# Kernel optimization log

Hardware: AMD Instinct MI355X
Metric: run time of the kernel (lower is better)

## Reference

```python
import jax, jax.numpy as jnp
import numpy as np
import math

NUM_HEADS = 32
NUM_KV = 8
D = 128          # num_hidden == per-head dim in this module
S = 2048
B = 1
DK = 128
ROPE_BASE = 10000.0


def rope(x):
    # x: [B, H, S, D]; standard Llama-style RoPE (split-halves rotation) over positions.
    d = x.shape[-1]
    half = d // 2
    pos = jnp.arange(x.shape[2], dtype=jnp.float32)                       # [S]
    inv_freq = 1.0 / (ROPE_BASE ** (jnp.arange(half, dtype=jnp.float32) / half))
    ang = pos[:, None] * inv_freq[None, :]                                # [S, half]
    cos = jnp.cos(ang)
    sin = jnp.sin(ang)
    x1 = x[..., :half]
    x2 = x[..., half:]
    return jnp.concatenate([x1 * cos - x2 * sin, x1 * sin + x2 * cos], axis=-1)


def setup_inputs() -> dict:
    key = jax.random.key(0)
    ks = jax.random.split(key, 8)
    query = jax.random.normal(ks[0], (B, S, D), dtype=jnp.float32)
    k_in = jax.random.normal(ks[1], (B, S, D), dtype=jnp.float32)
    v_in = jax.random.normal(ks[2], (B, S, D), dtype=jnp.float32)
    # causal mask: 1 where attention allowed (lower triangle incl diagonal)
    mask = jnp.tril(jnp.ones((S, S), dtype=jnp.int32))[None, None]        # [1,1,S,S]
    sc = 0.02
    Wq = jax.random.normal(ks[3], (NUM_HEADS * D, D), dtype=jnp.float32) * sc
    bq = jnp.zeros((NUM_HEADS * D,), dtype=jnp.float32)
    Wk = jax.random.normal(ks[4], (NUM_KV * D, D), dtype=jnp.float32) * sc
    bk = jnp.zeros((NUM_KV * D,), dtype=jnp.float32)
    Wv = jax.random.normal(ks[5], (NUM_KV * D, D), dtype=jnp.float32) * sc
    bv = jnp.zeros((NUM_KV * D,), dtype=jnp.float32)
    Wo = jax.random.normal(ks[6], (D, NUM_HEADS * D), dtype=jnp.float32) * sc
    bo = jnp.zeros((D,), dtype=jnp.float32)
    return {"query": query, "key": k_in, "values": v_in, "mask": mask,
            "Wq": Wq, "bq": bq, "Wk": Wk, "bk": bk, "Wv": Wv, "bv": bv,
            "Wo": Wo, "bo": bo}


def reference(query, key, values, mask, Wq, bq, Wk, bk, Wv, bv, Wo, bo):
    Bq, Sq, Dh = query.shape
    # projections; torch Linear: x @ W.T + b. Note: view (reshape), not transpose,
    # exactly as in the original module.
    q = (query @ Wq.T + bq).reshape(Bq, NUM_HEADS, Sq, Dh)   # [B,H,S,D]
    k = (key @ Wk.T + bk).reshape(Bq, NUM_KV, Sq, Dh)        # [B,Hkv,S,D]
    v = (values @ Wv.T + bv).reshape(Bq, NUM_KV, Sq, Dh)
    rk = rope(k)
    rv = rope(v)  # module applies RoPE to values too (faithful)
    rep = NUM_HEADS // NUM_KV
    # torch .repeat((1, rep, 1, 1)) tiles whole head blocks -> jnp.tile
    rk = jnp.tile(rk, (1, rep, 1, 1))                        # [B,H,S,D]
    rv = jnp.tile(rv, (1, rep, 1, 1))
    scores = jnp.einsum('bhqd,bhkd->bhqk', q, rk) / math.sqrt(DK)
    scores = jnp.where(mask == 0, -jnp.inf, scores)
    attn = jax.nn.softmax(scores, axis=-1)
    out = jnp.einsum('bhqk,bhkd->bhqd', attn, rv)            # [B,H,S,D]
    out = out.transpose(0, 2, 1, 3).reshape(Bq, Sq, NUM_HEADS * Dh)
    return out @ Wo.T + bo
```

## Files before the change

kernel.cpp:

```cpp
#include <hip/hip_runtime.h>

typedef unsigned short u16;
typedef unsigned int u32;
typedef short frag_t __attribute__((ext_vector_type(8)));
typedef float f32x4 __attribute__((ext_vector_type(4)));

#define S_LEN 2048

__device__ __forceinline__ float bf2f(u32 u) {
  union { u32 i; float f; } v; v.i = u << 16; return v.f;
}
__device__ __forceinline__ u16 f2bf(float f) {
  u32 x = __float_as_uint(f);
  u32 r = (x + 0x7fffu + ((x >> 16) & 1u)) >> 16;
  return (u16)r;
}
__device__ __forceinline__ u32 pkbf(float lo, float hi) {
  u32 r;
  asm("v_cvt_pk_bf16_f32 %0, %1, %2" : "=v"(r) : "v"(lo), "v"(hi));
  return r;
}
__device__ __forceinline__ void unpack8(uint4 r, float* o) {
  o[0] = bf2f(r.x & 0xffffu); o[1] = bf2f(r.x >> 16);
  o[2] = bf2f(r.y & 0xffffu); o[3] = bf2f(r.y >> 16);
  o[4] = bf2f(r.z & 0xffffu); o[5] = bf2f(r.z >> 16);
  o[6] = bf2f(r.w & 0xffffu); o[7] = bf2f(r.w >> 16);
}
__device__ __forceinline__ u16 ld_in(const void* p, size_t idx, bool fp32) {
  if (fp32) return f2bf(((const float*)p)[idx]);
  return ((const u16*)p)[idx];
}
__device__ __forceinline__ uint4 ld8(const void* p, size_t eidx, bool fp32) {
  if (!fp32) return *(const uint4*)((const u16*)p + eidx);
  const float4* f = (const float4*)((const float*)p + eidx);
  float4 x = f[0], y = f[1];
  uint4 r;
  r.x = pkbf(x.x, x.y);
  r.y = pkbf(x.z, x.w);
  r.z = pkbf(y.x, y.y);
  r.w = pkbf(y.z, y.w);
  return r;
}

__global__ __launch_bounds__(256) void proj_all(
    const void* __restrict__ query, const void* __restrict__ key,
    const void* __restrict__ values,
    const void* __restrict__ Wq, const void* __restrict__ bq,
    const void* __restrict__ Wk, const void* __restrict__ bk,
    const void* __restrict__ Wv, const void* __restrict__ bv,
    u16* __restrict__ Qb, u16* __restrict__ Kb, u16* __restrict__ Vtmp,
    u32* __restrict__ flag_out) {
  __shared__ u16 As[128][136];
  __shared__ u16 Ws[128][136];
  __shared__ u32 flagS;
  u16 (*Cs)[136] = As;
  const int t = threadIdx.x;
  if (t < 64) {
    u32 e = ((u32)((const u16*)query)[2 * t] >> 7) & 0xFFu;
    bool ok = (e >= 110u && e <= 140u);
    unsigned long long b = __ballot(ok);
    if (t == 0) flagS = (__popcll(b) < 32) ? 1u : 0u;
  }
  __syncthreads();
  const bool fp32 = (flagS != 0u);
  if (t == 0 && blockIdx.x == 0 && blockIdx.y == 0) *flag_out = flagS;
  const int x = blockIdx.x;
  const void *A, *W, *bias;
  u16* C; int N, n0;
  if (x < 32)      { A = query;  W = Wq; bias = bq; C = Qb;   N = 4096; n0 = x << 7; }
  else if (x < 40) { A = key;    W = Wk; bias = bk; C = Kb;   N = 1024; n0 = (x - 32) << 7; }
  else             { A = values; W = Wv; bias = bv; C = Vtmp; N = 1024; n0 = (x - 40) << 7; }
  const float osc = (x < 32) ? 0.12751743f : 1.0f;
  const int m0 = blockIdx.y << 7;
#pragma unroll
  for (int i = 0; i < 8; ++i) {
    int task = t + (i << 8);
    int row = task >> 4, ch = (task & 15) << 3;
    *(uint4*)&As[row][ch] = ld8(A, (size_t)(m0 + row) * 128 + ch, fp32);
    *(uint4*)&Ws[row][ch] = ld8(W, (size_t)(n0 + row) * 128 + ch, fp32);
  }
  __syncthreads();
  const int lane = t & 63, w = t >> 6, quad = lane >> 4, l15 = lane & 15;
  const int rm = (w & 1) << 6, rn = (w >> 1) << 6;
  f32x4 acc[4][4];
#pragma unroll
  for (int mt = 0; mt < 4; ++mt)
#pragma unroll
    for (int nt = 0; nt < 4; ++nt) acc[mt][nt] = 0.f;
#pragma unroll
  for (int mtp = 0; mtp < 2; ++mtp) {
    frag_t a0[4], a1[4];
#pragma unroll
    for (int kc = 0; kc < 4; ++kc) {
      a0[kc] = *(const frag_t*)&As[rm + mtp * 32 + l15][kc * 32 + quad * 8];
      a1[kc] = *(const frag_t*)&As[rm + mtp * 32 + 16 + l15][kc * 32 + quad * 8];
    }
#pragma unroll
    for (int nt = 0; nt < 4; ++nt)
#pragma unroll
      for (int kc = 0; kc < 4; ++kc) {
        frag_t b = *(const frag_t*)&Ws[rn + nt * 16 + l15][kc * 32 + quad * 8];
        acc[mtp * 2][nt] = __builtin_amdgcn_mfma_f32_16x16x32_bf16(a0[kc], b, acc[mtp * 2][nt], 0, 0, 0);
        acc[mtp * 2 + 1][nt] = __builtin_amdgcn_mfma_f32_16x16x32_bf16(a1[kc], b, acc[mtp * 2 + 1][nt], 0, 0, 0);
      }
  }
  __syncthreads();
#pragma unroll
  for (int nt = 0; nt < 4; ++nt) {
    float bb = bf2f((u32)ld_in(bias, n0 + rn + nt * 16 + l15, fp32));
#pragma unroll
    for (int mt = 0; mt < 4; ++mt) {
      int row = rm + ((mt >> 1) * 32) + ((mt & 1) * 16) + quad * 4;
#pragma unroll
      for (int r = 0; r < 4; ++r)
        Cs[row + r][rn + nt * 16 + l15] = f2bf((acc[mt][nt][r] + bb) * osc);
    }
  }
  __syncthreads();
#pragma unroll
  for (int i = 0; i < 8; ++i) {
    int task = t + (i << 8);
    int row = task >> 4, ch = (task & 15) << 3;
    *(uint4*)&C[(size_t)(m0 + row) * N + n0 + ch] = *(const uint4*)&Cs[row][ch];
  }
}

__global__ __launch_bounds__(256) void rope_kv_tr(u16* __restrict__ Kb,
                                                  const u16* __restrict__ Vb,
                                                  u16* __restrict__ VbT) {
  __shared__ u16 Lt[128][72];
  const int t = threadIdx.x;
  const int s0 = blockIdx.x << 6;
  const int g = blockIdx.y;
  for (int i = t; i < 4096; i += 256) {
    int s = s0 + (i >> 6), ii = i & 63;
    float invf = __expf(-(float)ii * 0.14391156831212787f);
    float ang = (float)s * invf;
    float sn, cs;
    sincosf(ang, &sn, &cs);
    size_t base = ((size_t)(g << 11) + s) * 128 + ii;
    float k1 = bf2f((u32)Kb[base]), k2 = bf2f((u32)Kb[base + 64]);
    Kb[base] = f2bf(k1 * cs - k2 * sn);
    Kb[base + 64] = f2bf(k1 * sn + k2 * cs);
  }
  const u16* src = Vb + (size_t)g * S_LEN * 128;
  for (int i = t; i < 512; i += 256) {
    int r = i >> 3, d8 = (i & 7) << 3;
    float lo[8], hi[8];
    unpack8(*(const uint4*)&src[(size_t)(s0 + r) * 128 + d8], lo);
    unpack8(*(const uint4*)&src[(size_t)(s0 + r) * 128 + d8 + 64], hi);
#pragma unroll
    for (int j = 0; j < 8; ++j) {
      float invf = __expf(-(float)(d8 + j) * 0.14391156831212787f);
      float ang = (float)(s0 + r) * invf;
      float sn, cs;
      sincosf(ang, &sn, &cs);
      Lt[d8 + j][r] = f2bf(lo[j] * cs - hi[j] * sn);
      Lt[d8 + 64 + j][r] = f2bf(lo[j] * sn + hi[j] * cs);
    }
  }
  __syncthreads();
  u16* dst = VbT + (size_t)g * 128 * S_LEN + s0;
  for (int i = t; i < 2048; i += 256) {
    int d = i >> 4, s4 = (i & 15) << 2;
    uint2 pk;
    pk.x = (u32)Lt[d][s4] | ((u32)Lt[d][s4 + 1] << 16);
    pk.y = (u32)Lt[d][s4 + 2] | ((u32)Lt[d][s4 + 3] << 16);
    *(uint2*)&dst[(size_t)d * S_LEN + s4] = pk;
  }
}

__global__ __launch_bounds__(256, 2) void attn_mfma(
    const u16* __restrict__ Qb, const u16* __restrict__ Kb,
    const u16* __restrict__ VbT, u16* __restrict__ OpA, u16* __restrict__ OpB,
    float2* __restrict__ Ml, int nkh) {
  __shared__ union SmemU {
    struct { u16 Kt[32][136]; u16 Vt[128][40]; u16 St[128][40]; } m;
    struct { u16 Og[128][136]; } e;
  } su;
  const int t = threadIdx.x;
  const int lane = t & 63, w = t >> 6, quad = lane >> 4, l15 = lane & 15;
  const int g = (int)blockIdx.x & 7;
  const int kh = (int)blockIdx.x >> 3;
  const int pi = (int)blockIdx.y;
  const int h = g + (w << 3);
  const u16* Kg = Kb + (size_t)g * S_LEN * 128;
  const u16* Vg = VbT + (size_t)g * 128 * S_LEN;
  const int kR = t >> 4, kC = (t & 15) << 3;
  const int vR = t >> 2, vC = (t & 3) << 3;
  u16* dst = kh ? OpB : OpA;

  for (int tp = 0; tp < 2; ++tp) {
    const int qt = tp ? pi : 63 - pi;
    const int q0 = qt << 5;
    const int niter = qt + 1;
    frag_t aq[2][4];
#pragma unroll
    for (int qp = 0; qp < 2; ++qp)
#pragma unroll
      for (int kc = 0; kc < 4; ++kc)
        aq[qp][kc] = *(const frag_t*)&Qb[((size_t)h * S_LEN + q0 + qp * 16 + l15) * 128 +
                                         kc * 32 + quad * 8];
    float m_r[2] = {-1e30f, -1e30f}, l_r[2] = {0.f, 0.f};
    f32x4 oacc[2][8];
#pragma unroll
    for (int qp = 0; qp < 2; ++qp)
#pragma unroll
      for (int nt = 0; nt < 8; ++nt) oacc[qp][nt] = 0.f;

    uint4 kpf[2], vpf[2];
    if (kh < niter) {
      const int k0 = kh << 5;
      kpf[0] = *(const uint4*)&Kg[(size_t)(k0 + kR) * 128 + kC];
      kpf[1] = *(const uint4*)&Kg[(size_t)(k0 + kR + 16) * 128 + kC];
      vpf[0] = *(const uint4*)&Vg[(size_t)vR * S_LEN + k0 + vC];
      vpf[1] = *(const uint4*)&Vg[(size_t)(vR + 64) * S_LEN + k0 + vC];
    }
    for (int sj = kh; sj < niter; sj += nkh) {
      const int k0 = sj << 5;
      __syncthreads();
      *(uint4*)&su.m.Kt[kR][kC] = kpf[0];
      *(uint4*)&su.m.Kt[kR + 16][kC] = kpf[1];
      *(uint4*)&su.m.Vt[vR][vC] = vpf[0];
      *(uint4*)&su.m.Vt[vR + 64][vC] = vpf[1];
      __syncthreads();
      if (sj + nkh < niter) {
        const int kn = (sj + nkh) << 5;
        kpf[0] = *(const uint4*)&Kg[(size_t)(kn + kR) * 128 + kC];
        kpf[1] = *(const uint4*)&Kg[(size_t)(kn + kR + 16) * 128 + kC];
        vpf[0] = *(const uint4*)&Vg[(size_t)vR * S_LEN + kn + vC];
        vpf[1] = *(const uint4*)&Vg[(size_t)(vR + 64) * S_LEN + kn + vC];
      }
      f32x4 s4[2][2];
#pragma unroll
      for (int kk = 0; kk < 2; ++kk) { s4[kk][0] = 0.f; s4[kk][1] = 0.f; }
#pragma unroll
      for (int kc = 0; kc < 4; ++kc)
#pragma unroll
        for (int kk = 0; kk < 2; ++kk) {
          frag_t a = *(const frag_t*)&su.m.Kt[kk * 16 + l15][kc * 32 + quad * 8];
          s4[kk][0] = __builtin_amdgcn_mfma_f32_16x16x32_bf16(a, aq[0][kc], s4[kk][0], 0, 0, 0);
          s4[kk][1] = __builtin_amdgcn_mfma_f32_16x16x32_bf16(a, aq[1][kc], s4[kk][1], 0, 0, 0);
        }
      const bool lastm = (sj == niter - 1);
      float alpha[2];
#pragma unroll
      for (int qp = 0; qp < 2; ++qp) {
        const int qg = q0 + qp * 16 + l15;
        float mx = -1e30f;
#pragma unroll
        for (int kk = 0; kk < 2; ++kk)
#pragma unroll
          for (int r = 0; r < 4; ++r) {
            float sv = s4[kk][qp][r];
            if (lastm && (k0 + kk * 16 + quad * 4 + r) > qg) sv = -1e30f;
            s4[kk][qp][r] = sv;
            mx = fmaxf(mx, sv);
          }
        mx = fmaxf(mx, __shfl_xor(mx, 16));
        mx = fmaxf(mx, __shfl_xor(mx, 32));
        float mn = fmaxf(m_r[qp], mx);
        alpha[qp] = __builtin_amdgcn_exp2f(m_r[qp] - mn);
        m_r[qp] = mn;
        float sum = 0.f;
        const int strow = w * 32 + qp * 16 + l15;
#pragma unroll
        for (int kk = 0; kk < 2; ++kk) {
          float p0 = __builtin_amdgcn_exp2f(s4[kk][qp][0] - mn);
          float p1 = __builtin_amdgcn_exp2f(s4[kk][qp][1] - mn);
          float p2 = __builtin_amdgcn_exp2f(s4[kk][qp][2] - mn);
          float p3 = __builtin_amdgcn_exp2f(s4[kk][qp][3] - mn);
          sum += (p0 + p1) + (p2 + p3);
          uint2 pk;
          pk.x = pkbf(p0, p1);
          pk.y = pkbf(p2, p3);
          *(uint2*)&su.m.St[strow][kk * 16 + quad * 4] = pk;
        }
        sum += __shfl_xor(sum, 16);
        sum += __shfl_xor(sum, 32);
        l_r[qp] = l_r[qp] * alpha[qp] + sum;
      }
      if (__any(alpha[0] < 1.0f || alpha[1] < 1.0f)) {
#pragma unroll
        for (int qp = 0; qp < 2; ++qp)
#pragma unroll
          for (int r = 0; r < 4; ++r) {
            float al = __shfl(alpha[qp], quad * 4 + r);
#pragma unroll
            for (int nt = 0; nt < 8; ++nt) oacc[qp][nt][r] *= al;
          }
      }
      frag_t pa0 = *(const frag_t*)&su.m.St[w * 32 + l15][quad * 8];
      frag_t pa1 = *(const frag_t*)&su.m.St[w * 32 + 16 + l15][quad * 8];
#pragma unroll
      for (int nt = 0; nt < 8; ++nt) {
        frag_t v = *(const frag_t*)&su.m.Vt[nt * 16 + l15][quad * 8];
        oacc[0][nt] = __builtin_amdgcn_mfma_f32_16x16x32_bf16(pa0, v, oacc[0][nt], 0, 0, 0);
        oacc[1][nt] = __builtin_amdgcn_mfma_f32_16x16x32_bf16(pa1, v, oacc[1][nt], 0, 0, 0);
      }
    }
    __syncthreads();
#pragma unroll
    for (int qp = 0; qp < 2; ++qp)
#pragma unroll
      for (int r = 0; r < 4; ++r) {
        float fac = 1.0f;
        if (nkh == 1) fac = 1.0f / __shfl(l_r[qp], quad * 4 + r);
        int row = w * 32 + qp * 16 + quad * 4 + r;
#pragma unroll
        for (int nt = 0; nt < 8; ++nt)
          su.e.Og[row][nt * 16 + l15] = f2bf(oacc[qp][nt][r] * fac);
      }
    __syncthreads();
#pragma unroll
    for (int jj = 0; jj < 8; ++jj) {
      int c = t + (jj << 8);
      int row = c >> 4, ch = (c & 15) << 3;
      int hh = row >> 5, qr = row & 31;
      *(uint4*)&dst[(size_t)(q0 + qr) * 4096 + (g + hh * 8) * 128 + ch] =
          *(const uint4*)&su.e.Og[row][ch];
    }
    if (nkh == 2 && quad == 0) {
#pragma unroll
      for (int qp = 0; qp < 2; ++qp)
        Ml[((size_t)kh * 32 + h) * S_LEN + q0 + qp * 16 + l15] =
            make_float2(m_r[qp], l_r[qp]);
    }
  }
}

__global__ __launch_bounds__(256) void out_part(
    const u16* __restrict__ OpA, const u16* __restrict__ OpB,
    const float2* __restrict__ Ml, const void* __restrict__ Wo,
    float* __restrict__ Pout, const u32* __restrict__ flagp, int nkh) {
  __shared__ u16 As[64][136];
  __shared__ u16 Ws[128][136];
  const bool fp32 = (*flagp != 0u);
  const int t = threadIdx.x;
  const int lane = t & 63, w = t >> 6, quad = lane >> 4, l15 = lane & 15;
  const int rm = (w & 1) << 5, rn = (w >> 1) << 6;
  const int m0 = (int)blockIdx.x << 6;
  const int z = (int)blockIdx.y;
  f32x4 acc[2][4];
#pragma unroll
  for (int mt = 0; mt < 2; ++mt)
#pragma unroll
    for (int nt = 0; nt < 4; ++nt) acc[mt][nt] = 0.f;
  for (int kc2 = 0; kc2 < 2; ++kc2) {
    if (kc2) __syncthreads();
    const int kc0 = (z << 8) + (kc2 << 7);
    const int hh = kc0 >> 7;
#pragma unroll
    for (int i = 0; i < 8; ++i) {
      int task = t + (i << 8);
      int row = task >> 4, ch = (task & 15) << 3;
      *(uint4*)&Ws[row][ch] = ld8(Wo, (size_t)row * 4096 + kc0 + ch, fp32);
    }
#pragma unroll
    for (int i = 0; i < 4; ++i) {
      int task = t + (i << 8);
      int row = task >> 4, ch = (task & 15) << 3;
      size_t idx = (size_t)(m0 + row) * 4096 + kc0 + ch;
      if (nkh == 2) {
        int s = m0 + row;
        float2 p1 = Ml[(size_t)hh * S_LEN + s];
        float2 p2 = Ml[(size_t)(32 + hh) * S_LEN + s];
        float mn = fmaxf(p1.x, p2.x);
        float a1 = __builtin_amdgcn_exp2f(p1.x - mn);
        float a2 = __builtin_amdgcn_exp2f(p2.x - mn);
        float linv = 1.0f / (a1 * p1.y + a2 * p2.y);
        float w1 = a1 * linv, w2 = a2 * linv;
        float o1[8], o2[8];
        unpack8(*(const uint4*)&OpA[idx], o1);
        unpack8(*(const uint4*)&OpB[idx], o2);
        uint4 r;
        r.x = pkbf(o1[0] * w1 + o2[0] * w2, o1[1] * w1 + o2[1] * w2);
        r.y = pkbf(o1[2] * w1 + o2[2] * w2, o1[3] * w1 + o2[3] * w2);
        r.z = pkbf(o1[4] * w1 + o2[4] * w2, o1[5] * w1 + o2[5] * w2);
        r.w = pkbf(o1[6] * w1 + o2[6] * w2, o1[7] * w1 + o2[7] * w2);
        *(uint4*)&As[row][ch] = r;
      } else {
        *(uint4*)&As[row][ch] = *(const uint4*)&OpA[idx];
      }
    }
    __syncthreads();
    frag_t a0[4], a1[4];
#pragma unroll
    for (int kc = 0; kc < 4; ++kc) {
      a0[kc] = *(const frag_t*)&As[rm + l15][kc * 32 + quad * 8];
      a1[kc] = *(const frag_t*)&As[rm + 16 + l15][kc * 32 + quad * 8];
    }
#pragma unroll
    for (int nt = 0; nt < 4; ++nt)
#pragma unroll
      for (int kc = 0; kc < 4; ++kc) {
        frag_t b = *(const frag_t*)&Ws[rn + nt * 16 + l15][kc * 32 + quad * 8];
        acc[0][nt] = __builtin_amdgcn_mfma_f32_16x16x32_bf16(a0[kc], b, acc[0][nt], 0, 0, 0);
        acc[1][nt] = __builtin_amdgcn_mfma_f32_16x16x32_bf16(a1[kc], b, acc[1][nt], 0, 0, 0);
      }
  }
#pragma unroll
  for (int mt = 0; mt < 2; ++mt) {
    int mrow = m0 + rm + mt * 16 + quad * 4;
#pragma unroll
    for (int nt = 0; nt < 4; ++nt) {
      int n = rn + nt * 16 + l15;
#pragma unroll
      for (int r = 0; r < 4; ++r)
        Pout[((size_t)z * 2048 + mrow + r) * 128 + n] = acc[mt][nt][r];
    }
  }
}

__global__ __launch_bounds__(256) void out_red(
    const float* __restrict__ Pout, const void* __restrict__ bo,
    void* __restrict__ out, const u32* __restrict__ flagp) {
  const bool fp32 = (*flagp != 0u);
  int e4 = blockIdx.x * 256 + threadIdx.x;
  const float4* P = (const float4*)Pout;
  float4 s = P[e4];
#pragma unroll
  for (int z = 1; z < 16; ++z) {
    float4 p = P[(size_t)z * 65536 + e4];
    s.x += p.x; s.y += p.y; s.z += p.z; s.w += p.w;
  }
  int n = (e4 << 2) & 127;
  s.x += bf2f((u32)ld_in(bo, n + 0, fp32));
  s.y += bf2f((u32)ld_in(bo, n + 1, fp32));
  s.z += bf2f((u32)ld_in(bo, n + 2, fp32));
  s.w += bf2f((u32)ld_in(bo, n + 3, fp32));
  if (fp32) {
    ((float4*)out)[e4] = s;
  } else {
    uint2 pk;
    pk.x = pkbf(s.x, s.y);
    pk.y = pkbf(s.z, s.w);
    *(uint2*)((u16*)out + (e4 << 2)) = pk;
  }
}

extern "C" void kernel_launch(void* const* d_in, const int* in_sizes, int n_in,
                              void* d_out, int out_size, void* d_ws, size_t ws_size,
                              hipStream_t stream) {
  (void)in_sizes; (void)n_in; (void)out_size;
  const void* query  = d_in[0];
  const void* key    = d_in[1];
  const void* values = d_in[2];
  const void* Wq = d_in[4];
  const void* bq = d_in[5];
  const void* Wk = d_in[6];
  const void* bk = d_in[7];
  const void* Wv = d_in[8];
  const void* bv = d_in[9];
  const void* Wo = d_in[10];
  const void* bo = d_in[11];

  char* ws = (char*)d_ws;
  u32* flag   = (u32*)ws;
  u16* Qb     = (u16*)(ws + 64);
  u16* Kb     = (u16*)(ws + 64 + (16ull << 20));
  u16* VbT    = (u16*)(ws + 64 + (20ull << 20));
  u16* Vtmp   = (u16*)(ws + 64 + (24ull << 20));
  u16* Ob     = (u16*)(ws + 64 + (24ull << 20));
  u16* OpB    = (u16*)(ws + 64 + (40ull << 20));
  float2* Mlb = (float2*)(ws + 64 + (56ull << 20));
  float* Pout = (float*)Qb;

  const bool split = (ws_size >= (58ull << 20));
  const int nkh = split ? 2 : 1;

  proj_all<<<dim3(48, 16), 256, 0, stream>>>(query, key, values, Wq, bq, Wk, bk,
                                             Wv, bv, Qb, Kb, Vtmp, flag);
  rope_kv_tr<<<dim3(32, 8), 256, 0, stream>>>(Kb, Vtmp, VbT);
  attn_mfma<<<dim3(8 * nkh, 32), 256, 0, stream>>>(Qb, Kb, VbT, Ob, OpB, Mlb, nkh);
  out_part<<<dim3(32, 16), 256, 0, stream>>>(Ob, OpB, Mlb, Wo, Pout, flag, nkh);
  out_red<<<256, 256, 0, stream>>>(Pout, bo, d_out, flag);
}
```

Measured before the change: 239.3 us.

## Fuse K RoPE into projection epilogue and allow 4-way KV split in attention

Applies RoPE to K inside the projection kernel's shared-memory epilogue instead of a separate read-modify-write pass in the V transpose kernel. The attention KV dimension can now be split four ways when the workspace is large enough, which doubles the attention grid. out_part merges up to four partial outputs using their saved max and sum statistics. The goal is better CU occupancy in attention and less K traffic, at the cost of more partial-output memory and merge work.

```diff
diff --git a/kernel.cpp b/kernel.cpp
--- a/kernel.cpp
+++ b/kernel.cpp
@@ -117,6 +117,21 @@
     }
   }
   __syncthreads();
+  if (x >= 32 && x < 40) {
+    const int g0 = x - 32;
+    for (int i = t; i < 8192; i += 256) {
+      int row = i >> 6, ii = i & 63;
+      int sv = (((m0 + row) & 255) << 3) + g0;
+      float invf = __expf(-(float)ii * 0.14391156831212787f);
+      float ang = (float)sv * invf;
+      float sn, cs;
+      sincosf(ang, &sn, &cs);
+      float k1 = bf2f((u32)Cs[row][ii]), k2 = bf2f((u32)Cs[row][ii + 64]);
+      Cs[row][ii] = f2bf(k1 * cs - k2 * sn);
+      Cs[row][ii + 64] = f2bf(k1 * sn + k2 * cs);
+    }
+    __syncthreads();
+  }
 #pragma unroll
   for (int i = 0; i < 8; ++i) {
     int task = t + (i << 8);
@@ -125,24 +140,12 @@
   }
 }
 
-__global__ __launch_bounds__(256) void rope_kv_tr(u16* __restrict__ Kb,
-                                                  const u16* __restrict__ Vb,
-                                                  u16* __restrict__ VbT) {
+__global__ __launch_bounds__(256) void rope_v_tr(const u16* __restrict__ Vb,
+                                                 u16* __restrict__ VbT) {
   __shared__ u16 Lt[128][72];
   const int t = threadIdx.x;
   const int s0 = blockIdx.x << 6;
   const int g = blockIdx.y;
-  for (int i = t; i < 4096; i += 256) {
-    int s = s0 + (i >> 6), ii = i & 63;
-    float invf = __expf(-(float)ii * 0.14391156831212787f);
-    float ang = (float)s * invf;
-    float sn, cs;
-    sincosf(ang, &sn, &cs);
-    size_t base = ((size_t)(g << 11) + s) * 128 + ii;
-    float k1 = bf2f((u32)Kb[base]), k2 = bf2f((u32)Kb[base + 64]);
-    Kb[base] = f2bf(k1 * cs - k2 * sn);
-    Kb[base + 64] = f2bf(k1 * sn + k2 * cs);
-  }
   const u16* src = Vb + (size_t)g * S_LEN * 128;
   for (int i = t; i < 512; i += 256) {
     int r = i >> 3, d8 = (i & 7) << 3;
@@ -172,7 +175,8 @@
 
 __global__ __launch_bounds__(256, 2) void attn_mfma(
     const u16* __restrict__ Qb, const u16* __restrict__ Kb,
-    const u16* __restrict__ VbT, u16* __restrict__ OpA, u16* __restrict__ OpB,
+    const u16* __restrict__ VbT, u16* __restrict__ Op0, u16* __restrict__ Op1,
+    u16* __restrict__ Op2, u16* __restrict__ Op3,
     float2* __restrict__ Ml, int nkh) {
   __shared__ union SmemU {
     struct { u16 Kt[32][136]; u16 Vt[128][40]; u16 St[128][40]; } m;
@@ -188,7 +192,7 @@
   const u16* Vg = VbT + (size_t)g * 128 * S_LEN;
   const int kR = t >> 4, kC = (t & 15) << 3;
   const int vR = t >> 2, vC = (t & 3) << 3;
-  u16* dst = kh ? OpB : OpA;
+  u16* dst = (kh == 0) ? Op0 : (kh == 1) ? Op1 : (kh == 2) ? Op2 : Op3;
 
   for (int tp = 0; tp < 2; ++tp) {
     const int qt = tp ? pi : 63 - pi;
@@ -320,7 +324,7 @@
       *(uint4*)&dst[(size_t)(q0 + qr) * 4096 + (g + hh * 8) * 128 + ch] =
           *(const uint4*)&su.e.Og[row][ch];
     }
-    if (nkh == 2 && quad == 0) {
+    if (nkh >= 2 && quad == 0) {
 #pragma unroll
       for (int qp = 0; qp < 2; ++qp)
         Ml[((size_t)kh * 32 + h) * S_LEN + q0 + qp * 16 + l15] =
@@ -330,7 +334,8 @@
 }
 
 __global__ __launch_bounds__(256) void out_part(
-    const u16* __restrict__ OpA, const u16* __restrict__ OpB,
+    const u16* __restrict__ Op0, const u16* __restrict__ Op1,
+    const u16* __restrict__ Op2, const u16* __restrict__ Op3,
     const float2* __restrict__ Ml, const void* __restrict__ Wo,
     float* __restrict__ Pout, const u32* __restrict__ flagp, int nkh) {
   __shared__ u16 As[64][136];
@@ -361,26 +366,50 @@
       int task = t + (i << 8);
       int row = task >> 4, ch = (task & 15) << 3;
       size_t idx = (size_t)(m0 + row) * 4096 + kc0 + ch;
-      if (nkh == 2) {
+      if (nkh >= 2) {
         int s = m0 + row;
-        float2 p1 = Ml[(size_t)hh * S_LEN + s];
-        float2 p2 = Ml[(size_t)(32 + hh) * S_LEN + s];
-        float mn = fmaxf(p1.x, p2.x);
+        float2 p0 = Ml[(size_t)hh * S_LEN + s];
+        float2 p1 = Ml[(size_t)(32 + hh) * S_LEN + s];
+        float mn = fmaxf(p0.x, p1.x);
+        float2 p2, p3;
+        if (nkh == 4) {
+          p2 = Ml[(size_t)(64 + hh) * S_LEN + s];
+          p3 = Ml[(size_t)(96 + hh) * S_LEN + s];
+          mn = fmaxf(mn, fmaxf(p2.x, p3.x));
+        }
+        float a0 = __builtin_amdgcn_exp2f(p0.x - mn);
         float a1 = __builtin_amdgcn_exp2f(p1.x - mn);
-        float a2 = __builtin_amdgcn_exp2f(p2.x - mn);
-        float linv = 1.0f / (a1 * p1.y + a2 * p2.y);
-        float w1 = a1 * linv, w2 = a2 * linv;
-        float o1[8], o2[8];
-        unpack8(*(const uint4*)&OpA[idx], o1);
-        unpack8(*(const uint4*)&OpB[idx], o2);
+        float lsum = a0 * p0.y + a1 * p1.y;
+        float a2 = 0.f, a3 = 0.f;
+        if (nkh == 4) {
+          a2 = __builtin_amdgcn_exp2f(p2.x - mn);
+          a3 = __builtin_amdgcn_exp2f(p3.x - mn);
+          lsum += a2 * p2.y + a3 * p3.y;
+        }
+        float linv = 1.0f / lsum;
+        float o[8], oi[8];
+        unpack8(*(const uint4*)&Op0[idx], o);
+#pragma unroll
+        for (int j = 0; j < 8; ++j) o[j] *= a0;
+        unpack8(*(const uint4*)&Op1[idx], oi);
+#pragma unroll
+        for (int j = 0; j < 8; ++j) o[j] += a1 * oi[j];
+        if (nkh == 4) {
+          unpack8(*(const uint4*)&Op2[idx], oi);
+#pragma unroll
+          for (int j = 0; j < 8; ++j) o[j] += a2 * oi[j];
+          unpack8(*(const uint4*)&Op3[idx], oi);
+#pragma unroll
+          for (int j = 0; j < 8; ++j) o[j] += a3 * oi[j];
+        }
         uint4 r;
-        r.x = pkbf(o1[0] * w1 + o2[0] * w2, o1[1] * w1 + o2[1] * w2);
-        r.y = pkbf(o1[2] * w1 + o2[2] * w2, o1[3] * w1 + o2[3] * w2);
-        r.z = pkbf(o1[4] * w1 + o2[4] * w2, o1[5] * w1 + o2[5] * w2);
-        r.w = pkbf(o1[6] * w1 + o2[6] * w2, o1[7] * w1 + o2[7] * w2);
+        r.x = pkbf(o[0] * linv, o[1] * linv);
+        r.y = pkbf(o[2] * linv, o[3] * linv);
+        r.z = pkbf(o[4] * linv, o[5] * linv);
+        r.w = pkbf(o[6] * linv, o[7] * linv);
         *(uint4*)&As[row][ch] = r;
       } else {
-        *(uint4*)&As[row][ch] = *(const uint4*)&OpA[idx];
+        *(uint4*)&As[row][ch] = *(const uint4*)&Op0[idx];
       }
     }
     __syncthreads();
@@ -461,18 +490,24 @@
   u16* Kb     = (u16*)(ws + 64 + (16ull << 20));
   u16* VbT    = (u16*)(ws + 64 + (20ull << 20));
   u16* Vtmp   = (u16*)(ws + 64 + (24ull << 20));
-  u16* Ob     = (u16*)(ws + 64 + (24ull << 20));
-  u16* OpB    = (u16*)(ws + 64 + (40ull << 20));
-  float2* Mlb = (float2*)(ws + 64 + (56ull << 20));
+  u16* Op0    = (u16*)(ws + 64 + (24ull << 20));
+  u16* Op1    = (u16*)(ws + 64 + (40ull << 20));
+  u16* Op2    = (u16*)(ws + 64 + (56ull << 20));
+  u16* Op3    = (u16*)(ws + 64 + (72ull << 20));
   float* Pout = (float*)Qb;
 
-  const bool split = (ws_size >= (58ull << 20));
-  const int nkh = split ? 2 : 1;
+  const bool s4w = (ws_size >= (91ull << 20));
+  const bool s2w = (ws_size >= (58ull << 20));
+  const int nkh = s4w ? 4 : (s2w ? 2 : 1);
+  float2* Mlb = (float2*)(s4w ? (ws + 64 + (88ull << 20))
+                              : (ws + 64 + (56ull << 20)));
 
   proj_all<<<dim3(48, 16), 256, 0, stream>>>(query, key, values, Wq, bq, Wk, bk,
                                              Wv, bv, Qb, Kb, Vtmp, flag);
-  rope_kv_tr<<<dim3(32, 8), 256, 0, stream>>>(Kb, Vtmp, VbT);
-  attn_mfma<<<dim3(8 * nkh, 32), 256, 0, stream>>>(Qb, Kb, VbT, Ob, OpB, Mlb, nkh);
-  out_part<<<dim3(32, 16), 256, 0, stream>>>(Ob, OpB, Mlb, Wo, Pout, flag, nkh);
+  rope_v_tr<<<dim3(32, 8), 256, 0, stream>>>(Vtmp, VbT);
+  attn_mfma<<<dim3(8 * nkh, 32), 256, 0, stream>>>(Qb, Kb, VbT, Op0, Op1, Op2,
+                                                   Op3, Mlb, nkh);
+  out_part<<<dim3(32, 16), 256, 0, stream>>>(Op0, Op1, Op2, Op3, Mlb, Wo, Pout,
+                                             flag, nkh);
   out_red<<<256, 256, 0, stream>>>(Pout, bo, d_out, flag);
 }
```

New measurement: 253.1 us. +5.8%, slower.

## Fuse K RoPE into projection epilogue and process two M tiles per block

Applied to the files above, without the earlier changes.

The projection kernel now handles two 128-row M tiles per block, loading the weight tile once and reusing it across both, with half as many blocks in the grid. RoPE for K is applied in shared memory inside the projection epilogue before the store, so the separate kernel no longer reads and rewrites K in global memory and now only rotates and transposes V. This cuts global traffic for K and repeated weight loads. In exchange the projection grid has fewer blocks (384) and K blocks carry extra sincos work, which may load-imbalance the launch.

```diff
diff --git a/kernel.cpp b/kernel.cpp
--- a/kernel.cpp
+++ b/kernel.cpp
@@ -71,78 +71,90 @@
   else if (x < 40) { A = key;    W = Wk; bias = bk; C = Kb;   N = 1024; n0 = (x - 32) << 7; }
   else             { A = values; W = Wv; bias = bv; C = Vtmp; N = 1024; n0 = (x - 40) << 7; }
   const float osc = (x < 32) ? 0.12751743f : 1.0f;
-  const int m0 = blockIdx.y << 7;
+  const bool isK = (x >= 32 && x < 40);
+  const int g0 = x - 32;
+  const int lane = t & 63, w = t >> 6, quad = lane >> 4, l15 = lane & 15;
+  const int rm = (w & 1) << 6, rn = (w >> 1) << 6;
 #pragma unroll
   for (int i = 0; i < 8; ++i) {
     int task = t + (i << 8);
     int row = task >> 4, ch = (task & 15) << 3;
-    *(uint4*)&As[row][ch] = ld8(A, (size_t)(m0 + row) * 128 + ch, fp32);
     *(uint4*)&Ws[row][ch] = ld8(W, (size_t)(n0 + row) * 128 + ch, fp32);
   }
-  __syncthreads();
-  const int lane = t & 63, w = t >> 6, quad = lane >> 4, l15 = lane & 15;
-  const int rm = (w & 1) << 6, rn = (w >> 1) << 6;
-  f32x4 acc[4][4];
-#pragma unroll
-  for (int mt = 0; mt < 4; ++mt)
-#pragma unroll
-    for (int nt = 0; nt < 4; ++nt) acc[mt][nt] = 0.f;
-#pragma unroll
-  for (int mtp = 0; mtp < 2; ++mtp) {
-    frag_t a0[4], a1[4];
-#pragma unroll
-    for (int kc = 0; kc < 4; ++kc) {
-      a0[kc] = *(const frag_t*)&As[rm + mtp * 32 + l15][kc * 32 + quad * 8];
-      a1[kc] = *(const frag_t*)&As[rm + mtp * 32 + 16 + l15][kc * 32 + quad * 8];
-    }
-#pragma unroll
-    for (int nt = 0; nt < 4; ++nt)
+  for (int mi = 0; mi < 2; ++mi) {
+    const int m0 = (((int)blockIdx.y << 1) | mi) << 7;
+    if (mi) __syncthreads();
+#pragma unroll
+    for (int i = 0; i < 8; ++i) {
+      int task = t + (i << 8);
+      int row = task >> 4, ch = (task & 15) << 3;
+      *(uint4*)&As[row][ch] = ld8(A, (size_t)(m0 + row) * 128 + ch, fp32);
+    }
+    __syncthreads();
+    f32x4 acc[4][4];
+#pragma unroll
+    for (int mt = 0; mt < 4; ++mt)
+#pragma unroll
+      for (int nt = 0; nt < 4; ++nt) acc[mt][nt] = 0.f;
+#pragma unroll
+    for (int mtp = 0; mtp < 2; ++mtp) {
+      frag_t a0[4], a1[4];
 #pragma unroll
       for (int kc = 0; kc < 4; ++kc) {
-        frag_t b = *(const frag_t*)&Ws[rn + nt * 16 + l15][kc * 32 + quad * 8];
-        acc[mtp * 2][nt] = __builtin_amdgcn_mfma_f32_16x16x32_bf16(a0[kc], b, acc[mtp * 2][nt], 0, 0, 0);
-        acc[mtp * 2 + 1][nt] = __builtin_amdgcn_mfma_f32_16x16x32_bf16(a1[kc], b, acc[mtp * 2 + 1][nt], 0, 0, 0);
-      }
-  }
-  __syncthreads();
-#pragma unroll
-  for (int nt = 0; nt < 4; ++nt) {
-    float bb = bf2f((u32)ld_in(bias, n0 + rn + nt * 16 + l15, fp32));
-#pragma unroll
-    for (int mt = 0; mt < 4; ++mt) {
-      int row = rm + ((mt >> 1) * 32) + ((mt & 1) * 16) + quad * 4;
-#pragma unroll
-      for (int r = 0; r < 4; ++r)
-        Cs[row + r][rn + nt * 16 + l15] = f2bf((acc[mt][nt][r] + bb) * osc);
-    }
-  }
-  __syncthreads();
-#pragma unroll
-  for (int i = 0; i < 8; ++i) {
-    int task = t + (i << 8);
-    int row = task >> 4, ch = (task & 15) << 3;
-    *(uint4*)&C[(size_t)(m0 + row) * N + n0 + ch] = *(const uint4*)&Cs[row][ch];
-  }
-}
-
-__global__ __launch_bounds__(256) void rope_kv_tr(u16* __restrict__ Kb,
-                                                  const u16* __restrict__ Vb,
-                                                  u16* __restrict__ VbT) {
+        a0[kc] = *(const frag_t*)&As[rm + mtp * 32 + l15][kc * 32 + quad * 8];
+        a1[kc] = *(const frag_t*)&As[rm + mtp * 32 + 16 + l15][kc * 32 + quad * 8];
+      }
+#pragma unroll
+      for (int nt = 0; nt < 4; ++nt)
+#pragma unroll
+        for (int kc = 0; kc < 4; ++kc) {
+          frag_t b = *(const frag_t*)&Ws[rn + nt * 16 + l15][kc * 32 + quad * 8];
+          acc[mtp * 2][nt] = __builtin_amdgcn_mfma_f32_16x16x32_bf16(a0[kc], b, acc[mtp * 2][nt], 0, 0, 0);
+          acc[mtp * 2 + 1][nt] = __builtin_amdgcn_mfma_f32_16x16x32_bf16(a1[kc], b, acc[mtp * 2 + 1][nt], 0, 0, 0);
+        }
+    }
+    __syncthreads();
+#pragma unroll
+    for (int nt = 0; nt < 4; ++nt) {
+      float bb = bf2f((u32)ld_in(bias, n0 + rn + nt * 16 + l15, fp32));
+#pragma unroll
+      for (int mt = 0; mt < 4; ++mt) {
+        int row = rm + ((mt >> 1) * 32) + ((mt & 1) * 16) + quad * 4;
+#pragma unroll
+        for (int r = 0; r < 4; ++r)
+          Cs[row + r][rn + nt * 16 + l15] = f2bf((acc[mt][nt][r] + bb) * osc);
+      }
+    }
+    __syncthreads();
+    if (isK) {
+      for (int i = t; i < 8192; i += 256) {
+        int row = i >> 6, ii = i & 63;
+        int sv = (((m0 + row) & 255) << 3) + g0;
+        float invf = __expf(-(float)ii * 0.14391156831212787f);
+        float ang = (float)sv * invf;
+        float sn, cs;
+        sincosf(ang, &sn, &cs);
+        float k1 = bf2f((u32)Cs[row][ii]), k2 = bf2f((u32)Cs[row][ii + 64]);
+        Cs[row][ii] = f2bf(k1 * cs - k2 * sn);
+        Cs[row][ii + 64] = f2bf(k1 * sn + k2 * cs);
+      }
+      __syncthreads();
+    }
+#pragma unroll
+    for (int i = 0; i < 8; ++i) {
+      int task = t + (i << 8);
+      int row = task >> 4, ch = (task & 15) << 3;
+      *(uint4*)&C[(size_t)(m0 + row) * N + n0 + ch] = *(const uint4*)&Cs[row][ch];
+    }
+  }
+}
+
+__global__ __launch_bounds__(256) void rope_v_tr(const u16* __restrict__ Vb,
+                                                 u16* __restrict__ VbT) {
   __shared__ u16 Lt[128][72];
   const int t = threadIdx.x;
   const int s0 = blockIdx.x << 6;
   const int g = blockIdx.y;
-  for (int i = t; i < 4096; i += 256) {
-    int s = s0 + (i >> 6), ii = i & 63;
-    float invf = __expf(-(float)ii * 0.14391156831212787f);
-    float ang = (float)s * invf;
-    float sn, cs;
-    sincosf(ang, &sn, &cs);
-    size_t base = ((size_t)(g << 11) + s) * 128 + ii;
-    float k1 = bf2f((u32)Kb[base]), k2 = bf2f((u32)Kb[base + 64]);
-    Kb[base] = f2bf(k1 * cs - k2 * sn);
-    Kb[base + 64] = f2bf(k1 * sn + k2 * cs);
-  }
   const u16* src = Vb + (size_t)g * S_LEN * 128;
   for (int i = t; i < 512; i += 256) {
     int r = i >> 3, d8 = (i & 7) << 3;
@@ -461,7 +473,7 @@
   u16* Kb     = (u16*)(ws + 64 + (16ull << 20));
   u16* VbT    = (u16*)(ws + 64 + (20ull << 20));
   u16* Vtmp   = (u16*)(ws + 64 + (24ull << 20));
-  u16* Ob     = (u16*)(ws + 64 + (24ull << 20));
+  u16* OpA    = (u16*)(ws + 64 + (24ull << 20));
   u16* OpB    = (u16*)(ws + 64 + (40ull << 20));
   float2* Mlb = (float2*)(ws + 64 + (56ull << 20));
   float* Pout = (float*)Qb;
@@ -469,10 +481,11 @@
   const bool split = (ws_size >= (58ull << 20));
   const int nkh = split ? 2 : 1;
 
-  proj_all<<<dim3(48, 16), 256, 0, stream>>>(query, key, values, Wq, bq, Wk, bk,
-                                             Wv, bv, Qb, Kb, Vtmp, flag);
-  rope_kv_tr<<<dim3(32, 8), 256, 0, stream>>>(Kb, Vtmp, VbT);
-  attn_mfma<<<dim3(8 * nkh, 32), 256, 0, stream>>>(Qb, Kb, VbT, Ob, OpB, Mlb, nkh);
-  out_part<<<dim3(32, 16), 256, 0, stream>>>(Ob, OpB, Mlb, Wo, Pout, flag, nkh);
+  proj_all<<<dim3(48, 8), 256, 0, stream>>>(query, key, values, Wq, bq, Wk, bk,
+                                            Wv, bv, Qb, Kb, Vtmp, flag);
+  rope_v_tr<<<dim3(32, 8), 256, 0, stream>>>(Vtmp, VbT);
+  attn_mfma<<<dim3(8 * nkh, 32), 256, 0, stream>>>(Qb, Kb, VbT, OpA, OpB, Mlb,
+                                                   nkh);
+  out_part<<<dim3(32, 16), 256, 0, stream>>>(OpA, OpB, Mlb, Wo, Pout, flag, nkh);
   out_red<<<256, 256, 0, stream>>>(Pout, bo, d_out, flag);
 }
```

Measured after the change: 236.2 us (median of 2 runs). About the same (-1.3%).
